# Performance work log

Measured on AMD Instinct MI355X. Metric: run time of the kernel, lower is better.

## Reference

```python
import jax, jax.numpy as jnp
import numpy as np

VOXEL_SIZE = (0.1, 0.1, 0.2)
PC_RANGE = (-51.2, -51.2, -5.0, 51.2, 51.2, 3.0)
B, N, C = 8, 1_000_000, 4


def setup_inputs() -> dict:
    key = jax.random.key(0)
    u = jax.random.uniform(key, (B, N, C), dtype=jnp.float32)
    # xyz spread slightly beyond the point-cloud range so some points are out-of-range;
    # 4th channel is an intensity in [0, 1].
    lo = jnp.array([-60.0, -60.0, -8.0, 0.0], jnp.float32)
    hi = jnp.array([60.0, 60.0, 6.0, 1.0], jnp.float32)
    pts = lo + u * (hi - lo)
    # inject NaNs to exercise the not_nan_mask path
    pts = pts.at[:, ::1000, 0].set(jnp.nan)
    return {"points": pts}


def reference(points):
    # Padded/masked equivalent of DynamicVoxelizer.forward.
    # Instead of stream-compacting each batch (dynamic shapes), we return
    # fixed-shape [B, N, ...] arrays plus a validity mask; invalid entries
    # carry the same sentinel (-1 coords / -1 idx) the torch code filters on.
    vs = jnp.array(VOXEL_SIZE, dtype=points.dtype)          # (3,) x,y,z
    rng = jnp.array(PC_RANGE, dtype=points.dtype)           # (6,)
    pmin = rng[:3]
    grid = jnp.round((rng[3:] - rng[:3]) / vs).astype(jnp.int32)  # (nx, ny, nz)

    xyz = points[..., :3]                                   # [B, N, 3]
    not_nan = ~jnp.isnan(points).any(axis=-1)               # [B, N]

    # dynamic voxelization (mmcv semantics, max_num_points=-1):
    # per-point integer voxel coordinate, -1 sentinel if out of grid.
    cf = jnp.floor((xyz - pmin) / vs)                       # [B, N, 3] float (x,y,z order)
    c = cf.astype(jnp.int32)
    in_range = ((c >= 0) & (c < grid)).all(axis=-1)         # [B, N]
    valid = not_nan & in_range                              # [B, N]

    # voxelizer returns coords in (z, y, x) order; -1 where invalid
    voxel_coords = jnp.where(valid[..., None], c[..., ::-1], -1)

    # _get_point_offsets: reorder zyx->xyz, center = coord*vs + min + vs/2
    centers = cf * vs + pmin + vs * 0.5                     # [B, N, 3]
    point_offsets = jnp.where(valid[..., None], xyz - centers, 0.0)

    point_idxes = jnp.where(valid, jnp.arange(N, dtype=jnp.int32)[None, :], -1)
    points_out = jnp.where(valid[..., None], points, 0.0)

    return points_out, voxel_coords, point_idxes, point_offsets, valid
```

## Files before the change

kernel.cpp:

```cpp
#include <hip/hip_runtime.h>


#define NPTS 1000000
#define BLK 128
#define WPT 256

typedef float f4 __attribute__((ext_vector_type(4)));

__global__ __launch_bounds__(BLK) void voxelize_kernel(
    const f4* __restrict__ pts, float* __restrict__ out, int total) {
  __shared__ __align__(16) float s_vox [2][WPT * 3];
  __shared__ __align__(16) float s_poff[2][WPT * 3];
  __shared__ __align__(16) float s_misc[2][WPT * 2];

  const int lane  = threadIdx.x & 63;
  const int wave  = threadIdx.x >> 6;
  const int pbase = blockIdx.x * ((BLK / 64) * WPT) + wave * WPT;

  f4 p[4];
#pragma unroll
  for (int k = 0; k < 4; ++k)
    p[k] = __builtin_nontemporal_load(&pts[pbase + k * 64 + lane]);

  float* sv = s_vox[wave];
  float* so = s_poff[wave];
  float* sm = s_misc[wave];

#pragma unroll
  for (int k = 0; k < 4; ++k) {
    const int i = pbase + k * 64 + lane;
    f4 q = p[k];
    bool has_nan = (q.x != q.x) | (q.y != q.y) | (q.z != q.z) | (q.w != q.w);

    float fx = floorf((q.x - (-51.2f)) / 0.1f);
    float fy = floorf((q.y - (-51.2f)) / 0.1f);
    float fz = floorf((q.z - (-5.0f))  / 0.2f);
    int cx = (int)fx, cy = (int)fy, cz = (int)fz;

    bool in_range = (cx >= 0) & (cx < 1024) &
                    (cy >= 0) & (cy < 1024) &
                    (cz >= 0) & (cz < 40);
    bool valid = (!has_nan) && in_range;

    float ox = q.x - (fx * 0.1f + (-51.2f) + 0.05f);
    float oy = q.y - (fy * 0.1f + (-51.2f) + 0.05f);
    float oz = q.z - (fz * 0.2f + (-5.0f)  + 0.1f);

    f4 po = valid ? q : (f4){0.0f, 0.0f, 0.0f, 0.0f};
    ((f4*)out)[i] = po;

    const int s = k * 64 + lane;
    sv[s * 3 + 0] = valid ? (float)cz : -1.0f;
    sv[s * 3 + 1] = valid ? (float)cy : -1.0f;
    sv[s * 3 + 2] = valid ? (float)cx : -1.0f;
    so[s * 3 + 0] = valid ? ox : 0.0f;
    so[s * 3 + 1] = valid ? oy : 0.0f;
    so[s * 3 + 2] = valid ? oz : 0.0f;
    sm[s]       = valid ? (float)(i % NPTS) : -1.0f;
    sm[WPT + s] = valid ? 1.0f : 0.0f;
  }

  __builtin_amdgcn_wave_barrier();

  const long long t = total;
  f4* gvox  = (f4*)(out + 4  * t) + (long long)pbase * 3 / 4;
  f4* gpoff = (f4*)(out + 8  * t) + (long long)pbase * 3 / 4;
  f4* gidx  = (f4*)(out + 7  * t) + pbase / 4;
  f4* gval  = (f4*)(out + 11 * t) + pbase / 4;

  const f4* v4 = (const f4*)sv;
  const f4* o4 = (const f4*)so;
  const f4* m4 = (const f4*)sm;

#pragma unroll
  for (int j = 0; j < 3; ++j) gvox[j * 64 + lane] = v4[j * 64 + lane];
#pragma unroll
  for (int j = 0; j < 3; ++j) gpoff[j * 64 + lane] = o4[j * 64 + lane];
  gidx[lane] = m4[lane];
  gval[lane] = m4[64 + lane];
}

__global__ __launch_bounds__(64) void voxelize_tail(
    const float* __restrict__ ptsf, float* __restrict__ out, int total, int start) {
  int i = start + blockIdx.x * blockDim.x + threadIdx.x;
  if (i >= total) return;
  float px = ptsf[i * 4 + 0], py = ptsf[i * 4 + 1];
  float pz = ptsf[i * 4 + 2], pw = ptsf[i * 4 + 3];
  bool has_nan = (px != px) | (py != py) | (pz != pz) | (pw != pw);
  float fx = floorf((px - (-51.2f)) / 0.1f);
  float fy = floorf((py - (-51.2f)) / 0.1f);
  float fz = floorf((pz - (-5.0f))  / 0.2f);
  int cx = (int)fx, cy = (int)fy, cz = (int)fz;
  bool in_range = (cx >= 0) & (cx < 1024) & (cy >= 0) & (cy < 1024) &
                  (cz >= 0) & (cz < 40);
  bool valid = (!has_nan) && in_range;
  float ox = px - (fx * 0.1f + (-51.2f) + 0.05f);
  float oy = py - (fy * 0.1f + (-51.2f) + 0.05f);
  float oz = pz - (fz * 0.2f + (-5.0f)  + 0.1f);
  long long t = total;
  out[i * 4 + 0] = valid ? px : 0.0f;
  out[i * 4 + 1] = valid ? py : 0.0f;
  out[i * 4 + 2] = valid ? pz : 0.0f;
  out[i * 4 + 3] = valid ? pw : 0.0f;
  float* vox  = out + 4 * t  + (long long)i * 3;
  float* poff = out + 8 * t  + (long long)i * 3;
  if (valid) {
    vox[0] = (float)cz; vox[1] = (float)cy; vox[2] = (float)cx;
    poff[0] = ox; poff[1] = oy; poff[2] = oz;
    out[7 * t + i]  = (float)(i % NPTS);
    out[11 * t + i] = 1.0f;
  } else {
    vox[0] = -1.0f; vox[1] = -1.0f; vox[2] = -1.0f;
    poff[0] = 0.0f; poff[1] = 0.0f; poff[2] = 0.0f;
    out[7 * t + i]  = -1.0f;
    out[11 * t + i] = 0.0f;
  }
}

extern "C" void kernel_launch(void* const* d_in, const int* in_sizes, int n_in,
                              void* d_out, int out_size, void* d_ws, size_t ws_size,
                              hipStream_t stream) {
  (void)n_in; (void)d_ws; (void)ws_size; (void)out_size;
  const f4* pts = (const f4*)d_in[0];
  float* out = (float*)d_out;
  int total = in_sizes[0] / 4;
  const int ppb = (BLK / 64) * WPT;
  int full_blocks = total / ppb;
  if (full_blocks > 0)
    voxelize_kernel<<<full_blocks, BLK, 0, stream>>>(pts, out, total);
  int rem = total - full_blocks * ppb;
  if (rem > 0)
    voxelize_tail<<<(rem + 63) / 64, 64, 0, stream>>>((const float*)d_in[0], out,
                                                      total, full_blocks * ppb);
}
```

Before: 451.0 us.

## Split voxelize kernel into two passes and drop nontemporal loads

```diff
diff --git a/kernel.cpp b/kernel.cpp
--- a/kernel.cpp
+++ b/kernel.cpp
@@ -7,10 +7,8 @@
 
 typedef float f4 __attribute__((ext_vector_type(4)));
 
-__global__ __launch_bounds__(BLK) void voxelize_kernel(
+__global__ __launch_bounds__(BLK) void voxelize_A(
     const f4* __restrict__ pts, float* __restrict__ out, int total) {
-  __shared__ __align__(16) float s_vox [2][WPT * 3];
-  __shared__ __align__(16) float s_poff[2][WPT * 3];
   __shared__ __align__(16) float s_misc[2][WPT * 2];
 
   const int lane  = threadIdx.x & 63;
@@ -20,10 +18,8 @@
   f4 p[4];
 #pragma unroll
   for (int k = 0; k < 4; ++k)
-    p[k] = __builtin_nontemporal_load(&pts[pbase + k * 64 + lane]);
+    p[k] = pts[pbase + k * 64 + lane];
 
-  float* sv = s_vox[wave];
-  float* so = s_poff[wave];
   float* sm = s_misc[wave];
 
 #pragma unroll
@@ -42,12 +38,59 @@
                     (cz >= 0) & (cz < 40);
     bool valid = (!has_nan) && in_range;
 
+    f4 po = valid ? q : (f4){0.0f, 0.0f, 0.0f, 0.0f};
+    ((f4*)out)[i] = po;
+
+    const int s = k * 64 + lane;
+    sm[s]       = valid ? (float)(i % NPTS) : -1.0f;
+    sm[WPT + s] = valid ? 1.0f : 0.0f;
+  }
+
+  __builtin_amdgcn_wave_barrier();
+
+  const long long t = total;
+  f4* gidx = (f4*)(out + 7  * t) + pbase / 4;
+  f4* gval = (f4*)(out + 11 * t) + pbase / 4;
+  const f4* m4 = (const f4*)sm;
+  gidx[lane] = m4[lane];
+  gval[lane] = m4[64 + lane];
+}
+
+__global__ __launch_bounds__(BLK) void voxelize_B(
+    const f4* __restrict__ pts, float* __restrict__ out, int total) {
+  __shared__ __align__(16) float s_vox [2][WPT * 3];
+  __shared__ __align__(16) float s_poff[2][WPT * 3];
+
+  const int lane  = threadIdx.x & 63;
+  const int wave  = threadIdx.x >> 6;
+  const int pbase = blockIdx.x * ((BLK / 64) * WPT) + wave * WPT;
+
+  f4 p[4];
+#pragma unroll
+  for (int k = 0; k < 4; ++k)
+    p[k] = pts[pbase + k * 64 + lane];
+
+  float* sv = s_vox[wave];
+  float* so = s_poff[wave];
+
+#pragma unroll
+  for (int k = 0; k < 4; ++k) {
+    f4 q = p[k];
+    bool has_nan = (q.x != q.x) | (q.y != q.y) | (q.z != q.z) | (q.w != q.w);
+
+    float fx = floorf((q.x - (-51.2f)) / 0.1f);
+    float fy = floorf((q.y - (-51.2f)) / 0.1f);
+    float fz = floorf((q.z - (-5.0f))  / 0.2f);
+    int cx = (int)fx, cy = (int)fy, cz = (int)fz;
+
+    bool in_range = (cx >= 0) & (cx < 1024) &
+                    (cy >= 0) & (cy < 1024) &
+                    (cz >= 0) & (cz < 40);
+    bool valid = (!has_nan) && in_range;
+
     float ox = q.x - (fx * 0.1f + (-51.2f) + 0.05f);
     float oy = q.y - (fy * 0.1f + (-51.2f) + 0.05f);
     float oz = q.z - (fz * 0.2f + (-5.0f)  + 0.1f);
-
-    f4 po = valid ? q : (f4){0.0f, 0.0f, 0.0f, 0.0f};
-    ((f4*)out)[i] = po;
 
     const int s = k * 64 + lane;
     sv[s * 3 + 0] = valid ? (float)cz : -1.0f;
@@ -56,28 +99,19 @@
     so[s * 3 + 0] = valid ? ox : 0.0f;
     so[s * 3 + 1] = valid ? oy : 0.0f;
     so[s * 3 + 2] = valid ? oz : 0.0f;
-    sm[s]       = valid ? (float)(i % NPTS) : -1.0f;
-    sm[WPT + s] = valid ? 1.0f : 0.0f;
   }
 
   __builtin_amdgcn_wave_barrier();
 
   const long long t = total;
-  f4* gvox  = (f4*)(out + 4  * t) + (long long)pbase * 3 / 4;
-  f4* gpoff = (f4*)(out + 8  * t) + (long long)pbase * 3 / 4;
-  f4* gidx  = (f4*)(out + 7  * t) + pbase / 4;
-  f4* gval  = (f4*)(out + 11 * t) + pbase / 4;
-
+  f4* gvox  = (f4*)(out + 4 * t) + (long long)pbase * 3 / 4;
+  f4* gpoff = (f4*)(out + 8 * t) + (long long)pbase * 3 / 4;
   const f4* v4 = (const f4*)sv;
   const f4* o4 = (const f4*)so;
-  const f4* m4 = (const f4*)sm;
-
 #pragma unroll
   for (int j = 0; j < 3; ++j) gvox[j * 64 + lane] = v4[j * 64 + lane];
 #pragma unroll
   for (int j = 0; j < 3; ++j) gpoff[j * 64 + lane] = o4[j * 64 + lane];
-  gidx[lane] = m4[lane];
-  gval[lane] = m4[64 + lane];
 }
 
 __global__ __launch_bounds__(64) void voxelize_tail(
@@ -126,8 +160,10 @@
   int total = in_sizes[0] / 4;
   const int ppb = (BLK / 64) * WPT;
   int full_blocks = total / ppb;
-  if (full_blocks > 0)
-    voxelize_kernel<<<full_blocks, BLK, 0, stream>>>(pts, out, total);
+  if (full_blocks > 0) {
+    voxelize_A<<<full_blocks, BLK, 0, stream>>>(pts, out, total);
+    voxelize_B<<<full_blocks, BLK, 0, stream>>>(pts, out, total);
+  }
   int rem = total - full_blocks * ppb;
   if (rem > 0)
     voxelize_tail<<<(rem + 63) / 64, 64, 0, stream>>>((const float*)d_in[0], out,
```

After: 484.0 us. 1.07x slower.
